# Kernel optimization log

Measured on AMD Instinct MI355X. Metric: run time of the kernel, lower is better.

The kernel has to match this reference:

```python
import jax, jax.numpy as jnp
import numpy as np

NUM_HEADS = 8
NUM_GROUPS = 32
EPS = 1e-5


def setup_inputs() -> dict:
    key = jax.random.key(0)
    ks = jax.random.split(key, 7)
    B, C, H, W = 8, 512, 32, 32
    x = jax.random.normal(ks[0], (B, C, H, W), dtype=jnp.float32)
    # GroupNorm affine params
    gn_w = jnp.ones((C,), dtype=jnp.float32)
    gn_b = jnp.zeros((C,), dtype=jnp.float32)
    # 1x1 conv == linear over channel dim; store squeezed weights (out, in)
    qkv_w = jax.random.normal(ks[1], (3 * C, C), dtype=jnp.float32) * (1.0 / np.sqrt(C))
    qkv_b = jnp.zeros((3 * C,), dtype=jnp.float32)
    proj_w = jax.random.normal(ks[2], (C, C), dtype=jnp.float32) * (1.0 / np.sqrt(C))
    proj_b = jnp.zeros((C,), dtype=jnp.float32)
    return {"x": x, "gn_w": gn_w, "gn_b": gn_b, "qkv_w": qkv_w,
            "qkv_b": qkv_b, "proj_w": proj_w, "proj_b": proj_b}


def reference(x, gn_w, gn_b, qkv_w, qkv_b, proj_w, proj_b):
    B, C, H, W = x.shape
    G = NUM_GROUPS
    hd = C // NUM_HEADS
    scale = hd ** -0.5
    # GroupNorm: normalize over (C//G, H, W) per group
    xg = x.reshape(B, G, C // G, H, W)
    mean = xg.mean(axis=(2, 3, 4), keepdims=True)
    var = xg.var(axis=(2, 3, 4), keepdims=True)
    xn = ((xg - mean) * jax.lax.rsqrt(var + EPS)).reshape(B, C, H, W)
    xn = xn * gn_w[None, :, None, None] + gn_b[None, :, None, None]
    # QKV 1x1 conv
    qkv = jnp.einsum('bchw,oc->bohw', xn, qkv_w) + qkv_b[None, :, None, None]
    # (B, 3, heads, head_dim, HW) -> (3, B, heads, HW, head_dim)
    qkv = qkv.reshape(B, 3, NUM_HEADS, hd, H * W).transpose(1, 0, 2, 4, 3)
    q, k, v = qkv[0], qkv[1], qkv[2]
    attn = jax.nn.softmax(jnp.einsum('bhqd,bhkd->bhqk', q, k) * scale, axis=-1)
    out = jnp.einsum('bhqk,bhkd->bhqd', attn, v)  # (B, heads, HW, hd)
    out = out.transpose(0, 1, 3, 2).reshape(B, C, H, W)
    out = jnp.einsum('bchw,oc->bohw', out, proj_w) + proj_b[None, :, None, None]
    return out + x
```

## Files before the change

kernel.cpp:

```cpp
#include <hip/hip_runtime.h>
#include <hip/hip_bf16.h>
#include <math.h>

typedef __bf16 bf16_t;
typedef __bf16 bf16x8 __attribute__((ext_vector_type(8)));
typedef __bf16 bf16x4 __attribute__((ext_vector_type(4)));
typedef float  f32x4  __attribute__((ext_vector_type(4)));
typedef short  short4v __attribute__((ext_vector_type(4)));

#define NB    8
#define NC    512
#define NHW   1024
#define NHEAD 8
#define NHD   64
#define NG    32
#define NCG   16
#define NO3   1536

__device__ __forceinline__ void lds_load16(bf16_t* lds, const bf16_t* g) {
  __builtin_amdgcn_global_load_lds(
      (__attribute__((address_space(1))) unsigned int*)(g),
      (__attribute__((address_space(3))) unsigned int*)(void*)(lds),
      16, 0, 0);
}

__device__ __forceinline__ f32x4 mfma16(bf16x4 a, bf16x4 b, f32x4 c) {
#if __has_builtin(__builtin_amdgcn_mfma_f32_16x16x16bf16_1k)
  return __builtin_amdgcn_mfma_f32_16x16x16bf16_1k(
      __builtin_bit_cast(short4v, a), __builtin_bit_cast(short4v, b), c, 0, 0, 0);
#else
  f32x4 d;
  asm("v_mfma_f32_16x16x16_bf16 %0, %1, %2, %3"
      : "=v"(d) : "v"(a), "v"(b), "v"(c));
  return d;
#endif
}

__global__ __launch_bounds__(256)
void gn_kernel(const float* __restrict__ x, const float* __restrict__ gw,
               const float* __restrict__ gb, bf16_t* __restrict__ xn)
{
  const int bg = blockIdx.x;
  const int b = bg >> 5, g = bg & 31;
  const float* xp = x + ((size_t)b * NC + g * NCG) * NHW;
  const int tid = threadIdx.x;
  const int wave = tid >> 6, lane = tid & 63;

  float s1 = 0.f, s2 = 0.f;
  const float4* xp4 = (const float4*)xp;
  for (int i = tid; i < 4096; i += 256) {
    float4 v = xp4[i];
    s1 += v.x + v.y + v.z + v.w;
    s2 += v.x * v.x + v.y * v.y + v.z * v.z + v.w * v.w;
  }
  for (int off = 32; off > 0; off >>= 1) {
    s1 += __shfl_down(s1, off);
    s2 += __shfl_down(s2, off);
  }
  __shared__ float red[16];
  if (lane == 0) { red[wave] = s1; red[8 + wave] = s2; }
  __syncthreads();
  float tot1 = red[0] + red[1] + red[2] + red[3];
  float tot2 = red[8] + red[9] + red[10] + red[11];
  const float mean = tot1 * (1.0f / 16384.0f);
  const float var  = tot2 * (1.0f / 16384.0f) - mean * mean;
  const float rstd = rsqrtf(var + 1e-5f);

  float gam[NCG], bet[NCG];
  #pragma unroll
  for (int c = 0; c < NCG; ++c) {
    gam[c] = gw[g * NCG + c] * rstd;
    bet[c] = gb[g * NCG + c] - mean * gam[c];
  }
  bf16_t* op = xn + (size_t)b * NHW * NC + g * NCG;
  for (int s = tid; s < NHW; s += 256) {
    __align__(16) bf16_t vals[NCG];
    #pragma unroll
    for (int c = 0; c < NCG; ++c)
      vals[c] = (bf16_t)(xp[c * NHW + s] * gam[c] + bet[c]);
    *(bf16x8*)(op + (size_t)s * NC)     = *(const bf16x8*)&vals[0];
    *(bf16x8*)(op + (size_t)s * NC + 8) = *(const bf16x8*)&vals[8];
  }
}

__global__ __launch_bounds__(256)
void wconv_kernel(const float* __restrict__ qw, const float* __restrict__ pw,
                  bf16_t* __restrict__ qwb, bf16_t* __restrict__ pwb)
{
  const int gid = blockIdx.x * 256 + threadIdx.x;
  const int n1 = NO3 * NC / 4;
  float4 v; bf16x4 o;
  if (gid < n1) {
    v = ((const float4*)qw)[gid];
    o[0] = (bf16_t)v.x; o[1] = (bf16_t)v.y; o[2] = (bf16_t)v.z; o[3] = (bf16_t)v.w;
    ((bf16x4*)qwb)[gid] = o;
  } else {
    int g2 = gid - n1;
    v = ((const float4*)pw)[g2];
    o[0] = (bf16_t)v.x; o[1] = (bf16_t)v.y; o[2] = (bf16_t)v.z; o[3] = (bf16_t)v.w;
    ((bf16x4*)pwb)[g2] = o;
  }
}

__device__ __forceinline__ void gemm_mainloop(const bf16_t* Ap, const bf16_t* Bp,
                                              bf16_t* sA, bf16_t* sB, f32x4 (&acc)[4][4])
{
  const int tid = threadIdx.x;
  const int wave = tid >> 6, lane = tid & 63;
  const int quad = lane >> 4, l16 = lane & 15;
  const int wm = wave >> 1, wn = wave & 1;
  for (int k0 = 0; k0 < 512; k0 += 32) {
    #pragma unroll
    for (int j = 0; j < 2; ++j) {
      int c = wave * 64 + j * 256 + lane;
      int row = c >> 2, ko = (c & 3) * 8;
      lds_load16(sA + (size_t)(wave * 64 + j * 256) * 8, Ap + (size_t)row * 512 + k0 + ko);
      lds_load16(sB + (size_t)(wave * 64 + j * 256) * 8, Bp + (size_t)row * 512 + k0 + ko);
    }
    __syncthreads();
    bf16x8 af[4], bfr[4];
    #pragma unroll
    for (int mi = 0; mi < 4; ++mi)
      af[mi] = *(const bf16x8*)(sA + (wm * 64 + mi * 16 + l16) * 32 + quad * 8);
    #pragma unroll
    for (int ni = 0; ni < 4; ++ni)
      bfr[ni] = *(const bf16x8*)(sB + (wn * 64 + ni * 16 + l16) * 32 + quad * 8);
    #pragma unroll
    for (int mi = 0; mi < 4; ++mi)
      #pragma unroll
      for (int ni = 0; ni < 4; ++ni)
        acc[mi][ni] = __builtin_amdgcn_mfma_f32_16x16x32_bf16(af[mi], bfr[ni], acc[mi][ni], 0, 0, 0);
    __syncthreads();
  }
}

__global__ __launch_bounds__(256, 2)
void qkv_gemm(const bf16_t* __restrict__ xn, const bf16_t* __restrict__ w,
              const float* __restrict__ bias,
              bf16_t* __restrict__ qbuf, bf16_t* __restrict__ kbuf, bf16_t* __restrict__ vbuf)
{
  __shared__ __align__(16) bf16_t smem[128 * 136];
  bf16_t* sA = smem;
  bf16_t* sB = smem + 4096;
  const int tid = threadIdx.x;
  const int wave = tid >> 6, lane = tid & 63;
  const int quad = lane >> 4, l16 = lane & 15;
  const int wm = wave >> 1, wn = wave & 1;
  const int bx = blockIdx.x, by = blockIdx.y, b = blockIdx.z;

  const bf16_t* Ap = xn + ((size_t)b * NHW + by * 128) * NC;
  const bf16_t* Bp = w + (size_t)bx * 128 * NC;
  f32x4 acc[4][4] = {};
  gemm_mainloop(Ap, Bp, sA, sB, acc);

  const int obase = bx * 128 + wn * 64;
  const int sbase = by * 128 + wm * 64;
  float bv[4];
  #pragma unroll
  for (int ni = 0; ni < 4; ++ni) bv[ni] = bias[obase + ni * 16 + l16];

  if (bx < 8) {
    const bool isq = (bx < 4);
    bf16_t* basep = isq ? qbuf : kbuf;
    const float scale = isq ? 0.125f : 1.0f;
    #pragma unroll
    for (int ni = 0; ni < 4; ++ni) {
      int o = obase + ni * 16 + l16;
      int hh = (o >> 6) & 7, dd = o & 63;
      bf16_t* dst = basep + ((size_t)(b * NHEAD + hh) * NHW) * NHD + dd;
      #pragma unroll
      for (int mi = 0; mi < 4; ++mi)
        #pragma unroll
        for (int r = 0; r < 4; ++r) {
          int s = sbase + mi * 16 + quad * 4 + r;
          dst[(size_t)s * NHD] = (bf16_t)((acc[mi][ni][r] + bv[ni]) * scale);
        }
    }
  } else {
    bf16_t* sC = smem;
    __syncthreads();
    #pragma unroll
    for (int ni = 0; ni < 4; ++ni)
      #pragma unroll
      for (int mi = 0; mi < 4; ++mi)
        #pragma unroll
        for (int r = 0; r < 4; ++r)
          sC[(wn * 64 + ni * 16 + l16) * 136 + wm * 64 + mi * 16 + quad * 4 + r] =
              (bf16_t)(acc[mi][ni][r] + bv[ni]);
    __syncthreads();
    int o_local = tid >> 1, shalf = (tid & 1) << 6;
    int ov = (bx - 8) * 128 + o_local;
    int hh = ov >> 6, dd = ov & 63;
    bf16_t* dst = vbuf + ((size_t)(b * NHEAD + hh) * NHD + dd) * NHW + by * 128 + shalf;
    #pragma unroll
    for (int jj = 0; jj < 8; ++jj)
      *(bf16x8*)(dst + jj * 8) = *(const bf16x8*)&sC[o_local * 136 + shalf + jj * 8];
  }
}

__global__ __launch_bounds__(256, 2)
void attn_kernel(const bf16_t* __restrict__ qbuf, const bf16_t* __restrict__ kbuf,
                 const bf16_t* __restrict__ vbuf, bf16_t* __restrict__ obuf)
{
  __shared__ __align__(16) bf16_t Ks[128 * 72];
  __shared__ __align__(16) bf16_t Vs[64 * 136];

  const int tid = threadIdx.x;
  const int wave = tid >> 6, lane = tid & 63;
  const int quad = lane >> 4, l16 = lane & 15;
  const int idx = blockIdx.x;
  const int qt = idx & 7, h = (idx >> 3) & 7, b = idx >> 6;
  const size_t bh = (size_t)b * NHEAD + h;
  const bf16_t* qp = qbuf + (bh * NHW + qt * 128 + wave * 32) * NHD;
  const bf16_t* kp = kbuf + bh * NHW * NHD;
  const bf16_t* vp = vbuf + bh * NHD * NHW;

  bf16x8 qf[2][2];
  #pragma unroll
  for (int stile = 0; stile < 2; ++stile)
    #pragma unroll
    for (int kc = 0; kc < 2; ++kc)
      qf[stile][kc] = *(const bf16x8*)(qp + (size_t)(stile * 16 + l16) * NHD + kc * 32 + quad * 8);

  float m_i[2] = {-1e30f, -1e30f}, l_i[2] = {0.f, 0.f};
  f32x4 oacc[4][2] = {};

  for (int kt = 0; kt < 8; ++kt) {
    const bf16_t* ksrc = kp + (size_t)kt * 128 * NHD;
    const bf16_t* vsrc = vp + kt * 128;
    #pragma unroll
    for (int j = 0; j < 4; ++j) {
      int c = tid + j * 256;
      int t = c >> 3, doff = (c & 7) * 8;
      *(bf16x8*)&Ks[t * 72 + doff] = *(const bf16x8*)(ksrc + (size_t)t * NHD + doff);
    }
    #pragma unroll
    for (int j = 0; j < 4; ++j) {
      int c = tid + j * 256;
      int d = c >> 4, toff = (c & 15) * 8;
      *(bf16x8*)&Vs[d * 136 + toff] = *(const bf16x8*)(vsrc + (size_t)d * NHW + toff);
    }
    __syncthreads();

    f32x4 st[2][8];
    #pragma unroll
    for (int mt = 0; mt < 8; ++mt) {
      bf16x8 ka0 = *(const bf16x8*)&Ks[(mt * 16 + l16) * 72 + quad * 8];
      bf16x8 ka1 = *(const bf16x8*)&Ks[(mt * 16 + l16) * 72 + 32 + quad * 8];
      #pragma unroll
      for (int stile = 0; stile < 2; ++stile) {
        f32x4 z = {};
        z = __builtin_amdgcn_mfma_f32_16x16x32_bf16(ka0, qf[stile][0], z, 0, 0, 0);
        z = __builtin_amdgcn_mfma_f32_16x16x32_bf16(ka1, qf[stile][1], z, 0, 0, 0);
        st[stile][mt] = z;
      }
    }

    #pragma unroll
    for (int stile = 0; stile < 2; ++stile) {
      float mx = -1e30f;
      #pragma unroll
      for (int mt = 0; mt < 8; ++mt)
        #pragma unroll
        for (int r = 0; r < 4; ++r) mx = fmaxf(mx, st[stile][mt][r]);
      mx = fmaxf(mx, __shfl_xor(mx, 16));
      mx = fmaxf(mx, __shfl_xor(mx, 32));
      float mnew = fmaxf(m_i[stile], mx);
      float alpha = __expf(m_i[stile] - mnew);
      m_i[stile] = mnew;
      float rs = 0.f;
      #pragma unroll
      for (int mt = 0; mt < 8; ++mt)
        #pragma unroll
        for (int r = 0; r < 4; ++r) {
          float p = __expf(st[stile][mt][r] - mnew);
          rs += p;
          st[stile][mt][r] = p;
        }
      rs += __shfl_xor(rs, 16);
      rs += __shfl_xor(rs, 32);
      l_i[stile] = l_i[stile] * alpha + rs;
      #pragma unroll
      for (int mi = 0; mi < 4; ++mi)
        #pragma unroll
        for (int r = 0; r < 4; ++r)
          oacc[mi][stile][r] *= alpha;
    }

    #pragma unroll
    for (int mt = 0; mt < 8; ++mt) {
      bf16x4 pb[2];
      #pragma unroll
      for (int stile = 0; stile < 2; ++stile) {
        pb[stile][0] = (bf16_t)st[stile][mt][0];
        pb[stile][1] = (bf16_t)st[stile][mt][1];
        pb[stile][2] = (bf16_t)st[stile][mt][2];
        pb[stile][3] = (bf16_t)st[stile][mt][3];
      }
      #pragma unroll
      for (int mi = 0; mi < 4; ++mi) {
        bf16x4 va = *(const bf16x4*)&Vs[(mi * 16 + l16) * 136 + mt * 16 + quad * 4];
        oacc[mi][0] = mfma16(va, pb[0], oacc[mi][0]);
        oacc[mi][1] = mfma16(va, pb[1], oacc[mi][1]);
      }
    }
    __syncthreads();
  }

  #pragma unroll
  for (int stile = 0; stile < 2; ++stile) {
    float inv = 1.0f / l_i[stile];
    int s = qt * 128 + wave * 32 + stile * 16 + l16;
    bf16_t* orow = obuf + ((size_t)b * NHW + s) * NC + h * NHD;
    #pragma unroll
    for (int mi = 0; mi < 4; ++mi) {
      __align__(8) bf16_t o4[4];
      #pragma unroll
      for (int r = 0; r < 4; ++r) o4[r] = (bf16_t)(oacc[mi][stile][r] * inv);
      *(bf16x4*)(orow + mi * 16 + quad * 4) = *(const bf16x4*)o4;
    }
  }
}

__global__ __launch_bounds__(256, 2)
void proj_gemm(const bf16_t* __restrict__ ob, const bf16_t* __restrict__ w,
               const float* __restrict__ bias, const float* __restrict__ x,
               float* __restrict__ out)
{
  __shared__ __align__(16) bf16_t smem[8192];
  bf16_t* sA = smem;
  bf16_t* sB = smem + 4096;
  const int tid = threadIdx.x;
  const int wave = tid >> 6, lane = tid & 63;
  const int quad = lane >> 4, l16 = lane & 15;
  const int wm = wave >> 1, wn = wave & 1;
  const int bx = blockIdx.x, by = blockIdx.y, b = blockIdx.z;

  const bf16_t* Ap = w + (size_t)by * 128 * NC;
  const bf16_t* Bp = ob + ((size_t)b * NHW + bx * 128) * NC;
  f32x4 acc[4][4] = {};
  gemm_mainloop(Ap, Bp, sA, sB, acc);

  const int cobase = by * 128 + wm * 64;
  const int sbase  = bx * 128 + wn * 64;
  #pragma unroll
  for (int mi = 0; mi < 4; ++mi)
    #pragma unroll
    for (int r = 0; r < 4; ++r) {
      int co = cobase + mi * 16 + quad * 4 + r;
      float pb = bias[co];
      const float* xrow = x + ((size_t)b * NC + co) * NHW;
      float* orow = out + ((size_t)b * NC + co) * NHW;
      #pragma unroll
      for (int ni = 0; ni < 4; ++ni) {
        int s = sbase + ni * 16 + l16;
        orow[s] = acc[mi][ni][r] + pb + xrow[s];
      }
    }
}

extern "C" void kernel_launch(void* const* d_in, const int* in_sizes, int n_in,
                              void* d_out, int out_size, void* d_ws, size_t ws_size,
                              hipStream_t stream)
{
  const float* x      = (const float*)d_in[0];
  const float* gn_w   = (const float*)d_in[1];
  const float* gn_b   = (const float*)d_in[2];
  const float* qkv_w  = (const float*)d_in[3];
  const float* qkv_b  = (const float*)d_in[4];
  const float* proj_w = (const float*)d_in[5];
  const float* proj_b = (const float*)d_in[6];
  float* out = (float*)d_out;

  char* ws = (char*)d_ws;
  bf16_t* xn   = (bf16_t*)(ws);
  bf16_t* qwb  = (bf16_t*)(ws + 8388608);
  bf16_t* pwb  = (bf16_t*)(ws + 9961472);
  bf16_t* qbuf = (bf16_t*)(ws + 10485760);
  bf16_t* kbuf = (bf16_t*)(ws + 18874368);
  bf16_t* vbuf = (bf16_t*)(ws + 27262976);
  bf16_t* obuf = xn;

  gn_kernel<<<dim3(NB * NG), dim3(256), 0, stream>>>(x, gn_w, gn_b, xn);
  wconv_kernel<<<dim3(1024), dim3(256), 0, stream>>>(qkv_w, proj_w, qwb, pwb);
  qkv_gemm<<<dim3(12, 8, NB), dim3(256), 0, stream>>>(xn, qwb, qkv_b, qbuf, kbuf, vbuf);
  attn_kernel<<<dim3(512), dim3(256), 0, stream>>>(qbuf, kbuf, vbuf, obuf);
  proj_gemm<<<dim3(8, 4, NB), dim3(256), 0, stream>>>(obuf, pwb, proj_b, x, out);
}
```

Baseline: 172.4 us.

## Split attention KV range across two wave groups and stage Q/K stores through LDS

The attention kernel now runs 512 threads per block, with two groups of four waves each handling half of the key tiles for the same query tile. The partial softmax states (m, l, O) are merged through LDS at the end. This doubles the parallelism per query tile and shortens each block's serial loop over key tiles, at the cost of an extra LDS merge and storing one partial O in bf16. Separately, the QKV GEMM now writes Q and K through an LDS transpose so the global stores are 16-byte vectors, and it folds log2(e) into the Q scale so the softmax can use exp2f.

```diff
diff --git a/kernel.cpp b/kernel.cpp
--- a/kernel.cpp
+++ b/kernel.cpp
@@ -16,6 +16,7 @@
 #define NG    32
 #define NCG   16
 #define NO3   1536
+#define LOG2E 1.4426950408889634f
 
 __device__ __forceinline__ void lds_load16(bf16_t* lds, const bf16_t* g) {
   __builtin_amdgcn_global_load_lds(
@@ -154,7 +155,6 @@
   gemm_mainloop(Ap, Bp, sA, sB, acc);
 
   const int obase = bx * 128 + wn * 64;
-  const int sbase = by * 128 + wm * 64;
   float bv[4];
   #pragma unroll
   for (int ni = 0; ni < 4; ++ni) bv[ni] = bias[obase + ni * 16 + l16];
@@ -162,20 +162,25 @@
   if (bx < 8) {
     const bool isq = (bx < 4);
     bf16_t* basep = isq ? qbuf : kbuf;
-    const float scale = isq ? 0.125f : 1.0f;
-    #pragma unroll
-    for (int ni = 0; ni < 4; ++ni) {
-      int o = obase + ni * 16 + l16;
-      int hh = (o >> 6) & 7, dd = o & 63;
-      bf16_t* dst = basep + ((size_t)(b * NHEAD + hh) * NHW) * NHD + dd;
+    const float scale = isq ? (0.125f * LOG2E) : 1.0f;
+    bf16_t* sC = smem;
+    __syncthreads();
+    #pragma unroll
+    for (int ni = 0; ni < 4; ++ni)
       #pragma unroll
       for (int mi = 0; mi < 4; ++mi)
         #pragma unroll
-        for (int r = 0; r < 4; ++r) {
-          int s = sbase + mi * 16 + quad * 4 + r;
-          dst[(size_t)s * NHD] = (bf16_t)((acc[mi][ni][r] + bv[ni]) * scale);
-        }
-    }
+        for (int r = 0; r < 4; ++r)
+          sC[(wm * 64 + mi * 16 + quad * 4 + r) * 136 + wn * 64 + ni * 16 + l16] =
+              (bf16_t)((acc[mi][ni][r] + bv[ni]) * scale);
+    __syncthreads();
+    int s_local = tid >> 1;
+    int ohalf = (tid & 1) << 6;
+    int hh = ((bx & 3) << 1) | (tid & 1);
+    bf16_t* dst = basep + (((size_t)(b * NHEAD + hh)) * NHW + by * 128 + s_local) * NHD;
+    #pragma unroll
+    for (int jj = 0; jj < 8; ++jj)
+      *(bf16x8*)(dst + jj * 8) = *(const bf16x8*)&sC[s_local * 136 + ohalf + jj * 8];
   } else {
     bf16_t* sC = smem;
     __syncthreads();
@@ -198,20 +203,23 @@
   }
 }
 
-__global__ __launch_bounds__(256, 2)
+__global__ __launch_bounds__(512, 4)
 void attn_kernel(const bf16_t* __restrict__ qbuf, const bf16_t* __restrict__ kbuf,
                  const bf16_t* __restrict__ vbuf, bf16_t* __restrict__ obuf)
 {
-  __shared__ __align__(16) bf16_t Ks[128 * 72];
-  __shared__ __align__(16) bf16_t Vs[64 * 136];
+  __shared__ __align__(16) bf16_t Ks[2][128 * 72];
+  __shared__ __align__(16) bf16_t Vs[2][64 * 136];
 
   const int tid = threadIdx.x;
   const int wave = tid >> 6, lane = tid & 63;
   const int quad = lane >> 4, l16 = lane & 15;
+  const int grp = wave >> 2;
+  const int wv = wave & 3;
+  const int tg = tid & 255;
   const int idx = blockIdx.x;
   const int qt = idx & 7, h = (idx >> 3) & 7, b = idx >> 6;
   const size_t bh = (size_t)b * NHEAD + h;
-  const bf16_t* qp = qbuf + (bh * NHW + qt * 128 + wave * 32) * NHD;
+  const bf16_t* qp = qbuf + (bh * NHW + qt * 128 + wv * 32) * NHD;
   const bf16_t* kp = kbuf + bh * NHW * NHD;
   const bf16_t* vp = vbuf + bh * NHD * NHW;
 
@@ -225,28 +233,29 @@
   float m_i[2] = {-1e30f, -1e30f}, l_i[2] = {0.f, 0.f};
   f32x4 oacc[4][2] = {};
 
-  for (int kt = 0; kt < 8; ++kt) {
+  for (int step = 0; step < 4; ++step) {
+    const int kt = grp * 4 + step;
     const bf16_t* ksrc = kp + (size_t)kt * 128 * NHD;
     const bf16_t* vsrc = vp + kt * 128;
     #pragma unroll
     for (int j = 0; j < 4; ++j) {
-      int c = tid + j * 256;
+      int c = tg + j * 256;
       int t = c >> 3, doff = (c & 7) * 8;
-      *(bf16x8*)&Ks[t * 72 + doff] = *(const bf16x8*)(ksrc + (size_t)t * NHD + doff);
+      *(bf16x8*)&Ks[grp][t * 72 + doff] = *(const bf16x8*)(ksrc + (size_t)t * NHD + doff);
     }
     #pragma unroll
     for (int j = 0; j < 4; ++j) {
-      int c = tid + j * 256;
+      int c = tg + j * 256;
       int d = c >> 4, toff = (c & 15) * 8;
-      *(bf16x8*)&Vs[d * 136 + toff] = *(const bf16x8*)(vsrc + (size_t)d * NHW + toff);
+      *(bf16x8*)&Vs[grp][d * 136 + toff] = *(const bf16x8*)(vsrc + (size_t)d * NHW + toff);
     }
     __syncthreads();
 
     f32x4 st[2][8];
     #pragma unroll
     for (int mt = 0; mt < 8; ++mt) {
-      bf16x8 ka0 = *(const bf16x8*)&Ks[(mt * 16 + l16) * 72 + quad * 8];
-      bf16x8 ka1 = *(const bf16x8*)&Ks[(mt * 16 + l16) * 72 + 32 + quad * 8];
+      bf16x8 ka0 = *(const bf16x8*)&Ks[grp][(mt * 16 + l16) * 72 + quad * 8];
+      bf16x8 ka1 = *(const bf16x8*)&Ks[grp][(mt * 16 + l16) * 72 + 32 + quad * 8];
       #pragma unroll
       for (int stile = 0; stile < 2; ++stile) {
         f32x4 z = {};
@@ -266,14 +275,14 @@
       mx = fmaxf(mx, __shfl_xor(mx, 16));
       mx = fmaxf(mx, __shfl_xor(mx, 32));
       float mnew = fmaxf(m_i[stile], mx);
-      float alpha = __expf(m_i[stile] - mnew);
+      float alpha = exp2f(m_i[stile] - mnew);
       m_i[stile] = mnew;
       float rs = 0.f;
       #pragma unroll
       for (int mt = 0; mt < 8; ++mt)
         #pragma unroll
         for (int r = 0; r < 4; ++r) {
-          float p = __expf(st[stile][mt][r] - mnew);
+          float p = exp2f(st[stile][mt][r] - mnew);
           rs += p;
           st[stile][mt][r] = p;
         }
@@ -299,7 +308,7 @@
       }
       #pragma unroll
       for (int mi = 0; mi < 4; ++mi) {
-        bf16x4 va = *(const bf16x4*)&Vs[(mi * 16 + l16) * 136 + mt * 16 + quad * 4];
+        bf16x4 va = *(const bf16x4*)&Vs[grp][(mi * 16 + l16) * 136 + mt * 16 + quad * 4];
         oacc[mi][0] = mfma16(va, pb[0], oacc[mi][0]);
         oacc[mi][1] = mfma16(va, pb[1], oacc[mi][1]);
       }
@@ -307,17 +316,43 @@
     __syncthreads();
   }
 
-  #pragma unroll
-  for (int stile = 0; stile < 2; ++stile) {
-    float inv = 1.0f / l_i[stile];
-    int s = qt * 128 + wave * 32 + stile * 16 + l16;
-    bf16_t* orow = obuf + ((size_t)b * NHW + s) * NC + h * NHD;
-    #pragma unroll
-    for (int mi = 0; mi < 4; ++mi) {
-      __align__(8) bf16_t o4[4];
-      #pragma unroll
-      for (int r = 0; r < 4; ++r) o4[r] = (bf16_t)(oacc[mi][stile][r] * inv);
-      *(bf16x4*)(orow + mi * 16 + quad * 4) = *(const bf16x4*)o4;
+  float* mlp = (float*)&Ks[1][0];
+  bf16_t* OL = &Vs[1][0];
+  if (grp == 1) {
+    #pragma unroll
+    for (int stile = 0; stile < 2; ++stile) {
+      int s_local = wv * 32 + stile * 16 + l16;
+      if (quad == 0) { mlp[s_local] = m_i[stile]; mlp[128 + s_local] = l_i[stile]; }
+      #pragma unroll
+      for (int mi = 0; mi < 4; ++mi) {
+        bf16x4 o4;
+        #pragma unroll
+        for (int r = 0; r < 4; ++r) o4[r] = (bf16_t)oacc[mi][stile][r];
+        *(bf16x4*)&OL[s_local * 68 + mi * 16 + quad * 4] = o4;
+      }
+    }
+  }
+  __syncthreads();
+  if (grp == 0) {
+    #pragma unroll
+    for (int stile = 0; stile < 2; ++stile) {
+      int s_local = wv * 32 + stile * 16 + l16;
+      float m2 = mlp[s_local], l2 = mlp[128 + s_local];
+      float m1 = m_i[stile], l1 = l_i[stile];
+      float mm = fmaxf(m1, m2);
+      float a1 = exp2f(m1 - mm), a2 = exp2f(m2 - mm);
+      float inv = 1.0f / (a1 * l1 + a2 * l2);
+      int s = qt * 128 + s_local;
+      bf16_t* orow = obuf + ((size_t)b * NHW + s) * NC + h * NHD;
+      #pragma unroll
+      for (int mi = 0; mi < 4; ++mi) {
+        bf16x4 o2 = *(const bf16x4*)&OL[s_local * 68 + mi * 16 + quad * 4];
+        __align__(8) bf16_t o4[4];
+        #pragma unroll
+        for (int r = 0; r < 4; ++r)
+          o4[r] = (bf16_t)((a1 * oacc[mi][stile][r] + a2 * (float)o2[r]) * inv);
+        *(bf16x4*)(orow + mi * 16 + quad * 4) = *(const bf16x4*)o4;
+      }
     }
   }
 }
@@ -384,6 +419,6 @@
   gn_kernel<<<dim3(NB * NG), dim3(256), 0, stream>>>(x, gn_w, gn_b, xn);
   wconv_kernel<<<dim3(1024), dim3(256), 0, stream>>>(qkv_w, proj_w, qwb, pwb);
   qkv_gemm<<<dim3(12, 8, NB), dim3(256), 0, stream>>>(xn, qwb, qkv_b, qbuf, kbuf, vbuf);
-  attn_kernel<<<dim3(512), dim3(256), 0, stream>>>(qbuf, kbuf, vbuf, obuf);
+  attn_kernel<<<dim3(512), dim3(512), 0, stream>>>(qbuf, kbuf, vbuf, obuf);
   proj_gemm<<<dim3(8, 4, NB), dim3(256), 0, stream>>>(obuf, pwb, proj_b, x, out);
 }
```

Result: slower. 233.6 us (+35.5%).
